# Performance work log

Measured on AMD Instinct MI355X. Metric: run time of the kernel, lower is better.

The kernel has to match this reference:

```python
import jax, jax.numpy as jnp
import numpy as np
import math

LMAX_IN = 3   # max l of the input SO3 vec arrays
LMIN, LMAX = 0, 3  # output l range from init args


def _cg_scalar(j1, m1, j2, m2, j, m):
    """Clebsch-Gordan coefficient <j1 m1 j2 m2 | j m> (real convention)."""
    if m1 + m2 != m:
        return 0.0
    f = math.factorial
    pref = math.sqrt((2 * j + 1) * f(j + j1 - j2) * f(j - j1 + j2) * f(j1 + j2 - j) / f(j1 + j2 + j + 1))
    pref *= math.sqrt(f(j + m) * f(j - m) * f(j1 + m1) * f(j1 - m1) * f(j2 + m2) * f(j2 - m2))
    s = 0.0
    for k in range(0, j1 + j2 - j + 1):
        d = [k, j1 + j2 - j - k, j1 - m1 - k, j2 + m2 - k, j - j2 + m1 + k, j - j1 - m2 + k]
        if any(x < 0 for x in d):
            continue
        denom = 1.0
        for x in d:
            denom *= float(f(x))
        s += (-1.0) ** k / denom
    return pref * s


def _cg_tensor(l1, l2, l):
    """Dense CG block C[M, m1, m2], shape (2l+1, 2l1+1, 2l2+1). Small, precomputed."""
    C = np.zeros((2 * l + 1, 2 * l1 + 1, 2 * l2 + 1), dtype=np.float32)
    for M in range(-l, l + 1):
        for m1 in range(-l1, l1 + 1):
            m2 = M - m1
            if abs(m2) <= l2:
                C[M + l, m1 + l1, m2 + l2] = _cg_scalar(l1, m1, l2, m2, l, M)
    return C

_CG_CACHE = {}

def _cg(l1, l2, l):
    key = (l1, l2, l)
    if key not in _CG_CACHE:
        _CG_CACHE[key] = jnp.asarray(_cg_tensor(l1, l2, l))
    return _CG_CACHE[key]


def _cg_product(A, B):
    """A, B: lists of [batch, 2l+1, tau] irrep features for l=0..LMAX_IN.
    Returns flattened concatenation over output l of [batch, 2l+1, tau_A*tau_B*npairs(l)]."""
    b = A[0].shape[0]
    outs = []
    for l in range(LMIN, LMAX + 1):
        parts = []
        for l1 in range(LMAX_IN + 1):
            for l2 in range(LMAX_IN + 1):
                if abs(l1 - l2) <= l <= l1 + l2:
                    # out[b,M,p,q] = sum_{m1,m2} CG[M,m1,m2] A[b,m1,p] B[b,m2,q]
                    blk = jnp.einsum('Mij,bip,bjq->bMpq', _cg(l1, l2, l), A[l1], B[l2])
                    parts.append(blk.reshape(b, 2 * l + 1, -1))
        outs.append(jnp.concatenate(parts, axis=-1))
    # pack the ragged per-l outputs into one flat array per batch element
    return jnp.concatenate([o.reshape(b, -1) for o in outs], axis=1)


def setup_inputs() -> dict:
    key = jax.random.key(0)
    ks = jax.random.split(key, 8)
    batch, tau = 4096, 16
    inp = {}
    for i, l in enumerate(range(LMAX_IN + 1)):
        inp[f'A{l}'] = jax.random.normal(ks[i], (batch, 2 * l + 1, tau), dtype=jnp.float32)
        inp[f'B{l}'] = jax.random.normal(ks[4 + i], (batch, 2 * l + 1, tau), dtype=jnp.float32)
    return inp


def reference(A0, A1, A2, A3, B0, B1, B2, B3):
    return _cg_product([A0, A1, A2, A3], [B0, B1, B2, B3])
```

## Files before the change

### kernel.cpp

```cpp
#include <hip/hip_runtime.h>

#define NTILES 156
#define NTERMS 478
#define PB_OUT 39936


constexpr double cfact(int n){ double f=1.0; for(int i=2;i<=n;++i) f*=(double)i; return f; }

constexpr double csqrt(double x){
  double g = (x > 1.0) ? x : 1.0;
  for (int i = 0; i < 32; ++i) g = 0.5*(g + x/g);
  return g;
}

constexpr double cg_coef(int j1,int m1,int j2,int m2,int j,int m){
  if (m1+m2 != m) return 0.0;
  double pref = csqrt((2.0*j+1.0)*cfact(j+j1-j2)*cfact(j-j1+j2)*cfact(j1+j2-j)/cfact(j1+j2+j+1));
  pref *= csqrt(cfact(j+m)*cfact(j-m)*cfact(j1+m1)*cfact(j1-m1)*cfact(j2+m2)*cfact(j2-m2));
  double s = 0.0;
  for (int k = 0; k <= j1+j2-j; ++k){
    int d2=j1+j2-j-k, d3=j1-m1-k, d4=j2+m2-k, d5=j-j2+m1+k, d6=j-j1-m2+k;
    if (d2<0||d3<0||d4<0||d5<0||d6<0) continue;
    double denom = cfact(k)*cfact(d2)*cfact(d3)*cfact(d4)*cfact(d5)*cfact(d6);
    s += ((k&1) ? -1.0 : 1.0)/denom;
  }
  return pref*s;
}

struct Tables {
  int   tiles[NTILES];
  int   tpack[NTERMS];
  float tcg[NTERMS];
};

constexpr Tables build_tables(){
  Tables t{};
  const int loff[4]   = {0,16,64,144};
  const int base[4]   = {0,1024,7936,22016};
  const int npairs[4] = {4,9,11,10};
  int tile_i = 0, term_i = 0;
  for (int l = 0; l <= 3; ++l){
    int pair_i = 0;
    for (int l1 = 0; l1 <= 3; ++l1){
      for (int l2 = 0; l2 <= 3; ++l2){
        int dl = l1 - l2; if (dl < 0) dl = -dl;
        if (!(dl <= l && l <= l1 + l2)) continue;
        for (int Mi = 0; Mi < 2*l + 1; ++Mi){
          int M = Mi - l;
          int m1lo = (-l1 > M - l2) ? -l1 : M - l2;
          int m1hi = ( l1 < M + l2) ?  l1 : M + l2;
          int cnt  = m1hi - m1lo + 1;
          int ooff = base[l] + (Mi*npairs[l] + pair_i)*256;
          t.tiles[tile_i] = ooff | (term_i << 16) | (cnt << 26);
          for (int m1 = m1lo; m1 <= m1hi; ++m1){
            int m2 = M - m1;
            t.tpack[term_i] = (loff[l1] + (m1 + l1)*16) | ((loff[l2] + (m2 + l2)*16) << 8);
            t.tcg[term_i]   = (float)cg_coef(l1, m1, l2, m2, l, M);
            ++term_i;
          }
          ++tile_i;
        }
        ++pair_i;
      }
    }
  }
  return t;
}

static constexpr Tables k_tab = build_tables();
__constant__ Tables g_tab = k_tab;

__global__ __launch_bounds__(256) void cg_main(
    const float* __restrict__ A0, const float* __restrict__ A1,
    const float* __restrict__ A2, const float* __restrict__ A3,
    const float* __restrict__ B0, const float* __restrict__ B1,
    const float* __restrict__ B2, const float* __restrict__ B3,
    float* __restrict__ out)
{
  __shared__ __align__(16) float Ash[256];
  __shared__ __align__(16) float Bsh[256];

  const int tid = threadIdx.x;
  const int b   = blockIdx.x;

  if (tid < 128){
    const bool isA = tid < 64;
    const int  i4  = (tid & 63) << 2;
    const float* src; int off;
    if      (i4 < 16)  { src = isA ? A0 : B0; off = b*16  + i4;       }
    else if (i4 < 64)  { src = isA ? A1 : B1; off = b*48  + i4 - 16;  }
    else if (i4 < 144) { src = isA ? A2 : B2; off = b*80  + i4 - 64;  }
    else               { src = isA ? A3 : B3; off = b*112 + i4 - 144; }
    const float4 v = *(const float4*)&src[off];
    float* dst = isA ? Ash : Bsh;
    *(float4*)&dst[i4] = v;
  }
  __syncthreads();

  const int lane = tid & 63;
  const int wv   = __builtin_amdgcn_readfirstlane(tid >> 6);
  const int p    = lane >> 2;
  const int q0   = (lane & 3) << 2;
  float* outb = out + (size_t)b * PB_OUT;

  for (int tg = 0; tg < NTILES; tg += 4){
    const int meta = g_tab.tiles[tg + wv];
    const int ooff = meta & 0xFFFF;
    const int ts   = (meta >> 16) & 0x3FF;
    const int tc   = meta >> 26;
    float4 acc = {0.f, 0.f, 0.f, 0.f};
    for (int i = 0; i < tc; ++i){
      const int   pk = g_tab.tpack[ts + i];
      const float cg = g_tab.tcg[ts + i];
      const float a  = Ash[(pk & 0xFF) + p];
      const float4 bq = *(const float4*)&Bsh[(pk >> 8) + q0];
      const float ca = cg * a;
      acc.x = fmaf(ca, bq.x, acc.x);
      acc.y = fmaf(ca, bq.y, acc.y);
      acc.z = fmaf(ca, bq.z, acc.z);
      acc.w = fmaf(ca, bq.w, acc.w);
    }
    *(float4*)&outb[ooff + (lane << 2)] = acc;
  }
}

extern "C" void kernel_launch(void* const* d_in, const int* in_sizes, int n_in,
                              void* d_out, int out_size, void* d_ws, size_t ws_size,
                              hipStream_t stream)
{
  const float* A0 = (const float*)d_in[0];
  const float* B0 = (const float*)d_in[1];
  const float* A1 = (const float*)d_in[2];
  const float* B1 = (const float*)d_in[3];
  const float* A2 = (const float*)d_in[4];
  const float* B2 = (const float*)d_in[5];
  const float* A3 = (const float*)d_in[6];
  const float* B3 = (const float*)d_in[7];
  float* out = (float*)d_out;

  const int batch = in_sizes[0] / 16;

  cg_main<<<batch, 256, 0, stream>>>(A0, A1, A2, A3, B0, B1, B2, B3, out);
}
```

Baseline: 666.7 us.

## Assign one batch element per wavefront with register-resident inputs and fully unrolled CG table

Each wavefront now handles a whole batch element instead of a block sharing one element across four waves. A and B rows are loaded straight into registers, removing the shared-memory staging and the barrier. The tile and term loops are fully unrolled at compile time, so CG coefficients and indices become immediates instead of constant-memory loads. The kernel is output-write bound (about 160 KB per element), so the gain may be limited, and the full unroll enlarges code size and register pressure.

```diff
diff --git a/kernel.cpp b/kernel.cpp
--- a/kernel.cpp
+++ b/kernel.cpp
@@ -1,9 +1,9 @@
 #include <hip/hip_runtime.h>
+#include <utility>
 
 #define NTILES 156
 #define NTERMS 478
 #define PB_OUT 39936
-
 
 constexpr double cfact(int n){ double f=1.0; for(int i=2;i<=n;++i) f*=(double)i; return f; }
 
@@ -68,60 +68,75 @@
 }
 
 static constexpr Tables k_tab = build_tables();
-__constant__ Tables g_tab = k_tab;
 
-__global__ __launch_bounds__(256) void cg_main(
+template <class F, int... Is>
+__device__ __forceinline__ void static_for_impl(F&& f, std::integer_sequence<int, Is...>){
+  ( f(std::integral_constant<int, Is>{}), ... );
+}
+template <int N, class F>
+__device__ __forceinline__ void static_for(F&& f){
+  static_for_impl(f, std::make_integer_sequence<int, N>{});
+}
+
+__global__ __launch_bounds__(256, 4) void cg_main(
     const float* __restrict__ A0, const float* __restrict__ A1,
     const float* __restrict__ A2, const float* __restrict__ A3,
     const float* __restrict__ B0, const float* __restrict__ B1,
     const float* __restrict__ B2, const float* __restrict__ B3,
-    float* __restrict__ out)
+    float* __restrict__ out, int batch)
 {
-  __shared__ __align__(16) float Ash[256];
-  __shared__ __align__(16) float Bsh[256];
-
-  const int tid = threadIdx.x;
-  const int b   = blockIdx.x;
-
-  if (tid < 128){
-    const bool isA = tid < 64;
-    const int  i4  = (tid & 63) << 2;
-    const float* src; int off;
-    if      (i4 < 16)  { src = isA ? A0 : B0; off = b*16  + i4;       }
-    else if (i4 < 64)  { src = isA ? A1 : B1; off = b*48  + i4 - 16;  }
-    else if (i4 < 144) { src = isA ? A2 : B2; off = b*80  + i4 - 64;  }
-    else               { src = isA ? A3 : B3; off = b*112 + i4 - 144; }
-    const float4 v = *(const float4*)&src[off];
-    float* dst = isA ? Ash : Bsh;
-    *(float4*)&dst[i4] = v;
-  }
-  __syncthreads();
-
+  const int tid  = threadIdx.x;
   const int lane = tid & 63;
   const int wv   = __builtin_amdgcn_readfirstlane(tid >> 6);
-  const int p    = lane >> 2;
-  const int q0   = (lane & 3) << 2;
-  float* outb = out + (size_t)b * PB_OUT;
+  const int b    = blockIdx.x * 4 + wv;
+  if (b >= batch) return;
 
-  for (int tg = 0; tg < NTILES; tg += 4){
-    const int meta = g_tab.tiles[tg + wv];
-    const int ooff = meta & 0xFFFF;
-    const int ts   = (meta >> 16) & 0x3FF;
-    const int tc   = meta >> 26;
+  const int p  = lane >> 2;
+  const int q0 = (lane & 3) << 2;
+
+  float  Arow[16];
+  float4 Bq[16];
+  static_for<16>([&](auto Rc){
+    constexpr int r = decltype(Rc)::value;
+    if constexpr (r == 0){
+      Arow[r] = A0[b*16 + p];
+      Bq[r]   = *(const float4*)&B0[b*16 + q0];
+    } else if constexpr (r < 4){
+      Arow[r] = A1[b*48 + (r-1)*16 + p];
+      Bq[r]   = *(const float4*)&B1[b*48 + (r-1)*16 + q0];
+    } else if constexpr (r < 9){
+      Arow[r] = A2[b*80 + (r-4)*16 + p];
+      Bq[r]   = *(const float4*)&B2[b*80 + (r-4)*16 + q0];
+    } else {
+      Arow[r] = A3[b*112 + (r-9)*16 + p];
+      Bq[r]   = *(const float4*)&B3[b*112 + (r-9)*16 + q0];
+    }
+  });
+
+  float* outb = out + (size_t)b * PB_OUT + (lane << 2);
+
+  static_for<NTILES>([&](auto Tc){
+    constexpr int ti   = decltype(Tc)::value;
+    constexpr int meta = k_tab.tiles[ti];
+    constexpr int ooff = meta & 0xFFFF;
+    constexpr int ts   = (meta >> 16) & 0x3FF;
+    constexpr int tc   = meta >> 26;
     float4 acc = {0.f, 0.f, 0.f, 0.f};
-    for (int i = 0; i < tc; ++i){
-      const int   pk = g_tab.tpack[ts + i];
-      const float cg = g_tab.tcg[ts + i];
-      const float a  = Ash[(pk & 0xFF) + p];
-      const float4 bq = *(const float4*)&Bsh[(pk >> 8) + q0];
-      const float ca = cg * a;
+    static_for<tc>([&](auto Jc){
+      constexpr int   j  = decltype(Jc)::value;
+      constexpr int   pk = k_tab.tpack[ts + j];
+      constexpr float cg = k_tab.tcg[ts + j];
+      constexpr int   ar = (pk & 0xFF) >> 4;
+      constexpr int   br = (pk >> 12);
+      const float  ca = cg * Arow[ar];
+      const float4 bq = Bq[br];
       acc.x = fmaf(ca, bq.x, acc.x);
       acc.y = fmaf(ca, bq.y, acc.y);
       acc.z = fmaf(ca, bq.z, acc.z);
       acc.w = fmaf(ca, bq.w, acc.w);
-    }
-    *(float4*)&outb[ooff + (lane << 2)] = acc;
-  }
+    });
+    *(float4*)(outb + ooff) = acc;
+  });
 }
 
 extern "C" void kernel_launch(void* const* d_in, const int* in_sizes, int n_in,
@@ -139,6 +154,7 @@
   float* out = (float*)d_out;
 
   const int batch = in_sizes[0] / 16;
+  const int grid  = (batch + 3) / 4;
 
-  cg_main<<<batch, 256, 0, stream>>>(A0, A1, A2, A3, B0, B1, B2, B3, out);
+  cg_main<<<grid, 256, 0, stream>>>(A0, A1, A2, A3, B0, B1, B2, B3, out, batch);
 }
```

Result: slower. 680.7 us (+2.1%).
